# Kernel optimization log

Hardware: AMD Instinct MI355X
Metric: run time of the kernel (lower is better)

The kernel has to match this reference:

```python
import jax, jax.numpy as jnp
import numpy as np

N = 100000
E = 3200000
F_IN, H1, H2, C = 256, 64, 32, 1000


def setup_inputs() -> dict:
    key = jax.random.key(0)
    ks = jax.random.split(key, 10)
    x = jax.random.normal(ks[0], (N, F_IN), dtype=jnp.float32)
    edge_src = jax.random.randint(ks[1], (E,), 0, N, dtype=jnp.int32)
    edge_dst = jax.random.randint(ks[2], (E,), 0, N, dtype=jnp.int32)
    s1 = 1.0 / np.sqrt(F_IN)
    s2 = 1.0 / np.sqrt(H1)
    s3 = 1.0 / np.sqrt(H2)
    W1 = jax.random.uniform(ks[3], (F_IN, H1), jnp.float32, -s1, s1)
    b1 = jnp.zeros((H1,), jnp.float32)
    W2 = jax.random.uniform(ks[4], (H1, H2), jnp.float32, -s2, s2)
    b2 = jnp.zeros((H2,), jnp.float32)
    Wfc = jax.random.uniform(ks[5], (H2, C), jnp.float32, -s3, s3)
    bfc = jax.random.uniform(ks[6], (C,), jnp.float32, -s3, s3)
    return {"x": x, "edge_src": edge_src, "edge_dst": edge_dst,
            "W1": W1, "b1": b1, "W2": W2, "b2": b2, "Wfc": Wfc, "bfc": bfc}


def _gcn_conv(x, W, b, src, dst, dinv):
    # PyG GCNConv: linear transform, then normalized scatter-add (with self-loops).
    xw = x @ W  # [N, out]
    coef = dinv[src] * dinv[dst]  # [E]
    msg = xw[src] * coef[:, None]  # gathered, scaled messages
    agg = jax.ops.segment_sum(msg, dst, num_segments=x.shape[0])
    agg = agg + xw * (dinv * dinv)[:, None]  # self-loop contribution
    return agg + b


def reference(x, edge_src, edge_dst, W1, b1, W2, b2, Wfc, bfc):
    n = x.shape[0]
    # degree with self-loops, counted on target nodes
    deg = 1.0 + jax.ops.segment_sum(jnp.ones_like(edge_dst, dtype=x.dtype), edge_dst, num_segments=n)
    dinv = jax.lax.rsqrt(deg)
    h = jax.nn.relu(_gcn_conv(x, W1, b1, edge_src, edge_dst, dinv))
    h = jax.nn.relu(_gcn_conv(h, W2, b2, edge_src, edge_dst, dinv))
    g = jnp.mean(h, axis=0)  # [H2]
    return g @ Wfc + bfc  # [C]
```

## Files before the change

kernel.cpp:

```cpp
#include <hip/hip_runtime.h>

#define N_NODES 100000
#define N_EDGES 3200000
#define F_IN 256
#define H1 64
#define H2 32
#define C_OUT 1000

#define OFF_G      0
#define OFF_DINV   64
#define OFF_HEAD   100096
#define OFF_NEXT   200128
#define OFF_Y1B    3400192
#define OFF_Y2B    6600192

__device__ __forceinline__ unsigned short f2bf(float f) {
    unsigned u = __float_as_uint(f);
    u += 0x7FFFu + ((u >> 16) & 1u);
    return (unsigned short)(u >> 16);
}
__device__ __forceinline__ float bf2f(unsigned short s) {
    return __uint_as_float(((unsigned)s) << 16);
}

__global__ void k_init(int* __restrict__ head, float* __restrict__ g) {
    int i = blockIdx.x * 256 + threadIdx.x;
    if (i < N_NODES) head[i] = -1;
    if (blockIdx.x == 0 && threadIdx.x < H2) g[threadIdx.x] = 0.0f;
}

__global__ void k_build(const int* __restrict__ dst, int* __restrict__ head,
                        int* __restrict__ next) {
    int e = blockIdx.x * 256 + threadIdx.x;
    if (e < N_EDGES) {
        int d = dst[e];
        int prev = atomicExch(&head[d], e);
        next[e] = prev;
    }
}

__global__ void k_deg(const int* __restrict__ head, const int* __restrict__ next,
                      float* __restrict__ dinv) {
    int n = blockIdx.x * 256 + threadIdx.x;
    if (n < N_NODES) {
        int cdeg = 0;
        int e = head[n];
        while (e >= 0) { cdeg++; e = next[e]; }
        dinv[n] = rsqrtf(1.0f + (float)cdeg);
    }
}

__global__ __launch_bounds__(256) void k_gemm1(const float* __restrict__ x,
                                               const float* __restrict__ W1,
                                               const float* __restrict__ dinv,
                                               unsigned short* __restrict__ y1b) {
    __shared__ float w[F_IN][H1];
    {
        const float4* Wv = (const float4*)W1;
        float4* wv = (float4*)&w[0][0];
        for (int i = threadIdx.x; i < F_IN * H1 / 4; i += 256) wv[i] = Wv[i];
    }
    __syncthreads();
    int n0 = blockIdx.x * 512 + threadIdx.x;
    int n1 = n0 + 256;
    bool v0 = n0 < N_NODES, v1 = n1 < N_NODES;
    int n0c = v0 ? n0 : 0, n1c = v1 ? n1 : 0;

    float acc0[H1], acc1[H1];
#pragma unroll
    for (int j = 0; j < H1; j++) { acc0[j] = 0.0f; acc1[j] = 0.0f; }

    const float4* xr0 = (const float4*)(x + (size_t)n0c * F_IN);
    const float4* xr1 = (const float4*)(x + (size_t)n1c * F_IN);
#pragma unroll 2
    for (int k0 = 0; k0 < F_IN / 4; k0++) {
        float4 xa = xr0[k0];
        float4 xb = xr1[k0];
#pragma unroll
        for (int d = 0; d < 4; d++) {
            float xv0 = (d == 0 ? xa.x : d == 1 ? xa.y : d == 2 ? xa.z : xa.w);
            float xv1 = (d == 0 ? xb.x : d == 1 ? xb.y : d == 2 ? xb.z : xb.w);
            const float4* wr = (const float4*)&w[k0 * 4 + d][0];
#pragma unroll
            for (int j4 = 0; j4 < H1 / 4; j4++) {
                float4 wq = wr[j4];
                acc0[j4 * 4 + 0] += xv0 * wq.x;
                acc0[j4 * 4 + 1] += xv0 * wq.y;
                acc0[j4 * 4 + 2] += xv0 * wq.z;
                acc0[j4 * 4 + 3] += xv0 * wq.w;
                acc1[j4 * 4 + 0] += xv1 * wq.x;
                acc1[j4 * 4 + 1] += xv1 * wq.y;
                acc1[j4 * 4 + 2] += xv1 * wq.z;
                acc1[j4 * 4 + 3] += xv1 * wq.w;
            }
        }
    }
    if (v0) {
        float dv = dinv[n0];
        unsigned pk[H1 / 2];
#pragma unroll
        for (int j2 = 0; j2 < H1 / 2; j2++) {
            unsigned lo = f2bf(acc0[2 * j2] * dv);
            unsigned hi = f2bf(acc0[2 * j2 + 1] * dv);
            pk[j2] = lo | (hi << 16);
        }
        uint4* o = (uint4*)(y1b + (size_t)n0 * H1);
#pragma unroll
        for (int q = 0; q < H1 / 8; q++)
            o[q] = make_uint4(pk[q * 4], pk[q * 4 + 1], pk[q * 4 + 2], pk[q * 4 + 3]);
    }
    if (v1) {
        float dv = dinv[n1];
        unsigned pk[H1 / 2];
#pragma unroll
        for (int j2 = 0; j2 < H1 / 2; j2++) {
            unsigned lo = f2bf(acc1[2 * j2] * dv);
            unsigned hi = f2bf(acc1[2 * j2 + 1] * dv);
            pk[j2] = lo | (hi << 16);
        }
        uint4* o = (uint4*)(y1b + (size_t)n1 * H1);
#pragma unroll
        for (int q = 0; q < H1 / 8; q++)
            o[q] = make_uint4(pk[q * 4], pk[q * 4 + 1], pk[q * 4 + 2], pk[q * 4 + 3]);
    }
}

__global__ __launch_bounds__(256) void k_agg1_gemm2(const unsigned short* __restrict__ y1b,
                                                    const int* __restrict__ head,
                                                    const int* __restrict__ next,
                                                    const int* __restrict__ src,
                                                    const float* __restrict__ dinv,
                                                    const float* __restrict__ b1,
                                                    const float* __restrict__ W2,
                                                    unsigned short* __restrict__ y2b) {
    __shared__ float w2s[H1][H2];
    __shared__ float hbuf[8][H1];
    {
        const float4* Wv = (const float4*)W2;
        float4* wv = (float4*)&w2s[0][0];
        for (int i = threadIdx.x; i < H1 * H2 / 4; i += 256) wv[i] = Wv[i];
    }

    const int t = threadIdx.x;
    const int wid = t >> 6;
    const int c = t & 63;
    const int n0 = blockIdx.x * 8 + wid * 2;
    const int n1 = n0 + 1;

    float a0 = bf2f(y1b[(size_t)n0 * H1 + c]);
    float a1 = bf2f(y1b[(size_t)n1 * H1 + c]);
    int e0 = head[n0], e1 = head[n1];
    while (e0 >= 0 && e1 >= 0) {
        int s0 = src[e0], s1 = src[e1];
        int t0 = next[e0], t1 = next[e1];
        a0 += bf2f(y1b[(size_t)s0 * H1 + c]);
        a1 += bf2f(y1b[(size_t)s1 * H1 + c]);
        e0 = t0; e1 = t1;
    }
    while (e0 >= 0) {
        int s0 = src[e0]; int t0 = next[e0];
        a0 += bf2f(y1b[(size_t)s0 * H1 + c]); e0 = t0;
    }
    while (e1 >= 0) {
        int s1 = src[e1]; int t1 = next[e1];
        a1 += bf2f(y1b[(size_t)s1 * H1 + c]); e1 = t1;
    }
    float h0 = dinv[n0] * a0 + b1[c];
    float h1v = dinv[n1] * a1 + b1[c];
    hbuf[wid * 2 + 0][c] = h0 > 0.0f ? h0 : 0.0f;
    hbuf[wid * 2 + 1][c] = h1v > 0.0f ? h1v : 0.0f;
    __syncthreads();

    {
        int w = t >> 5, j = t & 31;
        int n2 = blockIdx.x * 8 + w;
        float dot = 0.0f;
#pragma unroll
        for (int cc = 0; cc < H1; cc++) dot += hbuf[w][cc] * w2s[cc][j];
        y2b[(size_t)n2 * H2 + j] = f2bf(dinv[n2] * dot);
    }
}

__global__ __launch_bounds__(256) void k_agg2_pool(const unsigned short* __restrict__ y2b,
                                                   const int* __restrict__ head,
                                                   const int* __restrict__ next,
                                                   const int* __restrict__ src,
                                                   const float* __restrict__ dinv,
                                                   const float* __restrict__ b2,
                                                   float* __restrict__ g) {
    __shared__ float red[256];
    const int t = threadIdx.x;
    const int n = blockIdx.x * 8 + (t >> 5);
    const int c = t & 31;

    float a = bf2f(y2b[(size_t)n * H2 + c]);
    int e = head[n];
    while (e >= 0) {
        int s = src[e]; int nx = next[e];
        a += bf2f(y2b[(size_t)s * H2 + c]); e = nx;
    }
    float hv = dinv[n] * a + b2[c];
    red[t] = hv > 0.0f ? hv : 0.0f;
    __syncthreads();
    if (t < 128) red[t] += red[t + 128];
    __syncthreads();
    if (t < 64) red[t] += red[t + 64];
    __syncthreads();
    if (t < 32) {
        float s = red[t] + red[t + 32];
        atomicAdd(&g[t], s);
    }
}

__global__ void k_fc(const float* __restrict__ g, const float* __restrict__ Wfc,
                     const float* __restrict__ bfc, float* __restrict__ out) {
    int c = blockIdx.x * 256 + threadIdx.x;
    if (c < C_OUT) {
        const float invn = 1.0f / (float)N_NODES;
        float s = bfc[c];
#pragma unroll
        for (int k = 0; k < H2; k++) s += (g[k] * invn) * Wfc[k * C_OUT + c];
        out[c] = s;
    }
}

extern "C" void kernel_launch(void* const* d_in, const int* in_sizes, int n_in,
                              void* d_out, int out_size, void* d_ws, size_t ws_size,
                              hipStream_t stream) {
    const float* x   = (const float*)d_in[0];
    const int* esrc  = (const int*)d_in[1];
    const int* edst  = (const int*)d_in[2];
    const float* W1  = (const float*)d_in[3];
    const float* b1  = (const float*)d_in[4];
    const float* W2  = (const float*)d_in[5];
    const float* b2  = (const float*)d_in[6];
    const float* Wfc = (const float*)d_in[7];
    const float* bfc = (const float*)d_in[8];
    float* out = (float*)d_out;

    float* ws = (float*)d_ws;
    float* g    = ws + OFF_G;
    float* dinv = ws + OFF_DINV;
    int*   head = (int*)(ws + OFF_HEAD);
    int*   next = (int*)(ws + OFF_NEXT);
    unsigned short* y1b = (unsigned short*)(ws + OFF_Y1B);
    unsigned short* y2b = (unsigned short*)(ws + OFF_Y2B);

    const int nb_n = (N_NODES + 255) / 256;
    const int nb_e = (N_EDGES + 255) / 256;

    k_init<<<nb_n, 256, 0, stream>>>(head, g);
    k_build<<<nb_e, 256, 0, stream>>>(edst, head, next);
    k_deg<<<nb_n, 256, 0, stream>>>(head, next, dinv);

    k_gemm1<<<(N_NODES + 511) / 512, 256, 0, stream>>>(x, W1, dinv, y1b);
    k_agg1_gemm2<<<N_NODES / 8, 256, 0, stream>>>(y1b, head, next, esrc, dinv, b1, W2, y2b);
    k_agg2_pool<<<N_NODES / 8, 256, 0, stream>>>(y2b, head, next, esrc, dinv, b2, g);

    k_fc<<<(C_OUT + 255) / 256, 256, 0, stream>>>(g, Wfc, bfc, out);
}
```

Baseline: 856.2 us.

## Interleave src/next edge lists, count degrees atomically, store layer-2 features in FP8

Edge source and next-pointer are packed into one int2 array, so each linked-list hop does a single 8-byte load instead of two dependent loads from separate arrays. Degrees are now counted with atomicAdd while the list is built, which removes the separate pointer-chasing degree kernel. Layer-2 messages are stored as FP8 e4m3 and decoded through a shared-memory lookup table, halving gather bytes at the cost of precision. The FP8 rounding may break accuracy tolerances, and the extra atomic on cnt adds contention.

```diff
diff --git a/kernel.cpp b/kernel.cpp
--- a/kernel.cpp
+++ b/kernel.cpp
@@ -7,12 +7,13 @@
 #define H2 32
 #define C_OUT 1000
 
-#define OFF_G      0
-#define OFF_DINV   64
-#define OFF_HEAD   100096
-#define OFF_NEXT   200128
-#define OFF_Y1B    3400192
-#define OFF_Y2B    6600192
+#define OFF_G     0
+#define OFF_DINV  64
+#define OFF_CNT   100096
+#define OFF_HEAD  200128
+#define OFF_NODE2 300160
+#define OFF_Y1B   6700160
+#define OFF_Y2Q   9900160
 
 __device__ __forceinline__ unsigned short f2bf(float f) {
     unsigned u = __float_as_uint(f);
@@ -23,31 +24,56 @@
     return __uint_as_float(((unsigned)s) << 16);
 }
 
-__global__ void k_init(int* __restrict__ head, float* __restrict__ g) {
+__device__ __forceinline__ unsigned char f2fp8(float x) {
+    x = fminf(fmaxf(x, -448.0f), 448.0f);
+    unsigned u = __float_as_uint(x);
+    unsigned s = (u >> 24) & 0x80u;
+    unsigned absu = u & 0x7fffffffu;
+    float ax = __uint_as_float(absu);
+    if (ax < 0.015625f) {
+        int q = __float2int_rn(ax * 512.0f);
+        return (unsigned char)(s | (unsigned)q);
+    }
+    int e = (int)(absu >> 23) - 127;
+    unsigned man = absu & 0x7fffffu;
+    unsigned m3 = man >> 20;
+    unsigned rem = man & 0xFFFFFu;
+    if (rem > 0x80000u || (rem == 0x80000u && (m3 & 1u))) m3++;
+    if (m3 == 8u) { m3 = 0u; e++; }
+    if (e > 8) return (unsigned char)(s | 0x7Eu);
+    return (unsigned char)(s | ((unsigned)(e + 7) << 3) | m3);
+}
+
+__device__ __forceinline__ float fp8lut_val(int t) {
+    int ex = (t >> 3) & 15, man = t & 7;
+    int base = ex ? (8 + man) : man;
+    float v = ldexpf((float)base, (ex ? ex : 1) - 10);
+    return (t & 0x80) ? -v : v;
+}
+
+__global__ void k_init(int* __restrict__ head, int* __restrict__ cnt,
+                       float* __restrict__ g) {
     int i = blockIdx.x * 256 + threadIdx.x;
-    if (i < N_NODES) head[i] = -1;
+    if (i < N_NODES) { head[i] = -1; cnt[i] = 0; }
     if (blockIdx.x == 0 && threadIdx.x < H2) g[threadIdx.x] = 0.0f;
 }
 
-__global__ void k_build(const int* __restrict__ dst, int* __restrict__ head,
-                        int* __restrict__ next) {
+__global__ void k_build(const int* __restrict__ src, const int* __restrict__ dst,
+                        int* __restrict__ head, int* __restrict__ cnt,
+                        int2* __restrict__ node2) {
     int e = blockIdx.x * 256 + threadIdx.x;
     if (e < N_EDGES) {
         int d = dst[e];
+        int s = src[e];
         int prev = atomicExch(&head[d], e);
-        next[e] = prev;
-    }
-}
-
-__global__ void k_deg(const int* __restrict__ head, const int* __restrict__ next,
-                      float* __restrict__ dinv) {
+        node2[e] = make_int2(s, prev);
+        atomicAdd(&cnt[d], 1);
+    }
+}
+
+__global__ void k_dinv(const int* __restrict__ cnt, float* __restrict__ dinv) {
     int n = blockIdx.x * 256 + threadIdx.x;
-    if (n < N_NODES) {
-        int cdeg = 0;
-        int e = head[n];
-        while (e >= 0) { cdeg++; e = next[e]; }
-        dinv[n] = rsqrtf(1.0f + (float)cdeg);
-    }
+    if (n < N_NODES) dinv[n] = rsqrtf(1.0f + (float)cnt[n]);
 }
 
 __global__ __launch_bounds__(256) void k_gemm1(const float* __restrict__ x,
@@ -127,12 +153,11 @@
 
 __global__ __launch_bounds__(256) void k_agg1_gemm2(const unsigned short* __restrict__ y1b,
                                                     const int* __restrict__ head,
-                                                    const int* __restrict__ next,
-                                                    const int* __restrict__ src,
+                                                    const int2* __restrict__ node2,
                                                     const float* __restrict__ dinv,
                                                     const float* __restrict__ b1,
                                                     const float* __restrict__ W2,
-                                                    unsigned short* __restrict__ y2b) {
+                                                    unsigned char* __restrict__ y2q) {
     __shared__ float w2s[H1][H2];
     __shared__ float hbuf[8][H1];
     {
@@ -151,19 +176,21 @@
     float a1 = bf2f(y1b[(size_t)n1 * H1 + c]);
     int e0 = head[n0], e1 = head[n1];
     while (e0 >= 0 && e1 >= 0) {
-        int s0 = src[e0], s1 = src[e1];
-        int t0 = next[e0], t1 = next[e1];
-        a0 += bf2f(y1b[(size_t)s0 * H1 + c]);
-        a1 += bf2f(y1b[(size_t)s1 * H1 + c]);
-        e0 = t0; e1 = t1;
+        int2 v0 = node2[e0];
+        int2 v1 = node2[e1];
+        a0 += bf2f(y1b[(size_t)v0.x * H1 + c]);
+        a1 += bf2f(y1b[(size_t)v1.x * H1 + c]);
+        e0 = v0.y; e1 = v1.y;
     }
     while (e0 >= 0) {
-        int s0 = src[e0]; int t0 = next[e0];
-        a0 += bf2f(y1b[(size_t)s0 * H1 + c]); e0 = t0;
+        int2 v0 = node2[e0];
+        a0 += bf2f(y1b[(size_t)v0.x * H1 + c]);
+        e0 = v0.y;
     }
     while (e1 >= 0) {
-        int s1 = src[e1]; int t1 = next[e1];
-        a1 += bf2f(y1b[(size_t)s1 * H1 + c]); e1 = t1;
+        int2 v1 = node2[e1];
+        a1 += bf2f(y1b[(size_t)v1.x * H1 + c]);
+        e1 = v1.y;
     }
     float h0 = dinv[n0] * a0 + b1[c];
     float h1v = dinv[n1] * a1 + b1[c];
@@ -177,27 +204,31 @@
         float dot = 0.0f;
 #pragma unroll
         for (int cc = 0; cc < H1; cc++) dot += hbuf[w][cc] * w2s[cc][j];
-        y2b[(size_t)n2 * H2 + j] = f2bf(dinv[n2] * dot);
-    }
-}
-
-__global__ __launch_bounds__(256) void k_agg2_pool(const unsigned short* __restrict__ y2b,
+        y2q[(size_t)n2 * H2 + j] = f2fp8(dinv[n2] * dot);
+    }
+}
+
+__global__ __launch_bounds__(256) void k_agg2_pool(const unsigned char* __restrict__ y2q,
                                                    const int* __restrict__ head,
-                                                   const int* __restrict__ next,
-                                                   const int* __restrict__ src,
+                                                   const int2* __restrict__ node2,
                                                    const float* __restrict__ dinv,
                                                    const float* __restrict__ b2,
                                                    float* __restrict__ g) {
+    __shared__ float lut[256];
     __shared__ float red[256];
     const int t = threadIdx.x;
+    lut[t] = fp8lut_val(t);
+    __syncthreads();
+
     const int n = blockIdx.x * 8 + (t >> 5);
     const int c = t & 31;
 
-    float a = bf2f(y2b[(size_t)n * H2 + c]);
+    float a = lut[y2q[(size_t)n * H2 + c]];
     int e = head[n];
     while (e >= 0) {
-        int s = src[e]; int nx = next[e];
-        a += bf2f(y2b[(size_t)s * H2 + c]); e = nx;
+        int2 v = node2[e];
+        a += lut[y2q[(size_t)v.x * H2 + c]];
+        e = v.y;
     }
     float hv = dinv[n] * a + b2[c];
     red[t] = hv > 0.0f ? hv : 0.0f;
@@ -241,21 +272,22 @@
     float* ws = (float*)d_ws;
     float* g    = ws + OFF_G;
     float* dinv = ws + OFF_DINV;
+    int*   cnt  = (int*)(ws + OFF_CNT);
     int*   head = (int*)(ws + OFF_HEAD);
-    int*   next = (int*)(ws + OFF_NEXT);
+    int2*  node2 = (int2*)(ws + OFF_NODE2);
     unsigned short* y1b = (unsigned short*)(ws + OFF_Y1B);
-    unsigned short* y2b = (unsigned short*)(ws + OFF_Y2B);
+    unsigned char*  y2q = (unsigned char*)(ws + OFF_Y2Q);
 
     const int nb_n = (N_NODES + 255) / 256;
     const int nb_e = (N_EDGES + 255) / 256;
 
-    k_init<<<nb_n, 256, 0, stream>>>(head, g);
-    k_build<<<nb_e, 256, 0, stream>>>(edst, head, next);
-    k_deg<<<nb_n, 256, 0, stream>>>(head, next, dinv);
+    k_init<<<nb_n, 256, 0, stream>>>(head, cnt, g);
+    k_build<<<nb_e, 256, 0, stream>>>(esrc, edst, head, cnt, node2);
+    k_dinv<<<nb_n, 256, 0, stream>>>(cnt, dinv);
 
     k_gemm1<<<(N_NODES + 511) / 512, 256, 0, stream>>>(x, W1, dinv, y1b);
-    k_agg1_gemm2<<<N_NODES / 8, 256, 0, stream>>>(y1b, head, next, esrc, dinv, b1, W2, y2b);
-    k_agg2_pool<<<N_NODES / 8, 256, 0, stream>>>(y2b, head, next, esrc, dinv, b2, g);
+    k_agg1_gemm2<<<N_NODES / 8, 256, 0, stream>>>(y1b, head, node2, dinv, b1, W2, y2q);
+    k_agg2_pool<<<N_NODES / 8, 256, 0, stream>>>(y2q, head, node2, dinv, b2, g);
 
     k_fc<<<(C_OUT + 255) / 256, 256, 0, stream>>>(g, Wfc, bfc, out);
 }
```

Result: slower. 969.9 us (+13.3%).
